# Performance work log

Hardware: AMD Instinct MI355X
Metric: run time of the kernel (lower is better)

Reference implementation:

```python
import jax, jax.numpy as jnp
import numpy as np

B, C, H, W = 2, 1024, 64, 64
E, TOP_K = 8, 2
FFN = C  # ffn_dim = in_channels; hidden_dim = out_channels = in_channels


def setup_inputs() -> dict:
    key = jax.random.key(0)
    ks = jax.random.split(key, 5)
    s = 0.02
    return {
        "hidden_states": jax.random.normal(ks[0], (B, C, H, W), jnp.float32),
        "gate_w": jax.random.normal(ks[1], (E, C), jnp.float32) * s,   # torch Linear weight [out,in]
        "w1": jax.random.normal(ks[2], (E, FFN, C), jnp.float32) * s,
        "w2": jax.random.normal(ks[3], (E, C, FFN), jnp.float32) * s,
        "w3": jax.random.normal(ks[4], (E, FFN, C), jnp.float32) * s,
    }


def reference(hidden_states, gate_w, w1, w2, w3):
    b, c = hidden_states.shape[0], hidden_states.shape[1]
    space = hidden_states.shape[2:]
    # (B, C, H, W) -> (B, H, W, C) -> (T, C)
    x = jnp.transpose(hidden_states, (0, 2, 3, 1)).reshape(-1, c)

    # Router: softmax in float32, top-k, renormalize (matches torch)
    logits = x @ gate_w.T                                   # [T, E]
    probs = jax.nn.softmax(logits.astype(jnp.float32), axis=-1)
    rw, sel = jax.lax.top_k(probs, TOP_K)                   # [T, K]
    rw = rw / jnp.sum(rw, axis=-1, keepdims=True)
    rw = rw.astype(x.dtype)

    # Combine weights per expert: zero where expert not selected -> exact
    # equivalence with gather/scatter dispatch (full capacity, no drops).
    combine = jnp.sum(jax.nn.one_hot(sel, E, dtype=x.dtype) * rw[..., None], axis=1)  # [T, E]

    out = jnp.zeros_like(x)
    for e in range(E):  # small fixed expert loop
        h = jax.nn.gelu(x @ w1[e].T, approximate=False) * (x @ w3[e].T)  # SwiGLU-style [T, FFN]
        out = out + combine[:, e:e + 1] * (h @ w2[e].T)

    out = out.reshape(b, *space, c)
    return jnp.transpose(out, (0, 3, 1, 2))  # (B, C, H, W)
```

## Files before the change

kernel.cpp:

```cpp
#include <hip/hip_runtime.h>
#include <hip/hip_bf16.h>
#include <math.h>

#define BB 2
#define CC 1024
#define HH 64
#define WW 64
#define HWH (HH*WW)
#define TT (BB*HWH)
#define EE 8
#define FFN 1024
#define MAXTILES 71
#define HCAP (MAXTILES*256)

typedef __bf16 bf16x8 __attribute__((ext_vector_type(8)));
typedef float  f32x4  __attribute__((ext_vector_type(4)));

__device__ __forceinline__ void gl_lds16(const __bf16* g, __bf16* l) {
    __builtin_amdgcn_global_load_lds(
        (const __attribute__((address_space(1))) void*)g,
        (__attribute__((address_space(3))) void*)l, 16, 0, 0);
}

__device__ __forceinline__ void barrier_raw() {
    asm volatile("" ::: "memory");
    __builtin_amdgcn_s_barrier();
    asm volatile("" ::: "memory");
}

__device__ __forceinline__ int xcd_swz(int orig, int nwg) {
    const int q = nwg >> 3, r = nwg & 7, x = orig & 7, o8 = orig >> 3;
    return (x < r ? x * (q + 1) : r * (q + 1) + (x - r) * q) + o8;
}

__device__ __forceinline__ float gelu_fast(float a) {
    const float a2 = a * a;
    const float t  = a * fmaf(0.044715f, a2, 1.0f);
    const float u  = __builtin_amdgcn_exp2f(t * -2.30220795f);
    return a * __builtin_amdgcn_rcpf(1.0f + u);
}

#define WAITV(N) asm volatile("s_waitcnt vmcnt(" #N ")" ::: "memory")
#define LGKM0()  asm volatile("s_waitcnt lgkmcnt(0)" ::: "memory")
#define SCHED0() __builtin_amdgcn_sched_barrier(0)
#define PRIO1()  __builtin_amdgcn_s_setprio(1)
#define PRIO0()  __builtin_amdgcn_s_setprio(0)

#define CVB 12288
#define XPB 8192
#define RTB 512
__global__ __launch_bounds__(256) void k_prep(
    const float* __restrict__ hs, const float* __restrict__ gate_w,
    const float* __restrict__ w1, const float* __restrict__ w2,
    const float* __restrict__ w3,
    __bf16* __restrict__ w1b, __bf16* __restrict__ w2b,
    __bf16* __restrict__ w3b, __bf16* __restrict__ X,
    float* __restrict__ logP) {
    __shared__ float sm[2112];
    const int bid = blockIdx.x;
    const int tid = threadIdx.x;

    if (bid < CVB) {
        const float* s; __bf16* d; int lb = bid;
        if (lb < 4096)      { s = w1; d = w1b; }
        else if (lb < 8192) { s = w2; d = w2b; lb -= 4096; }
        else                { s = w3; d = w3b; lb -= 8192; }
        const size_t i = (size_t)lb * 2048 + (size_t)tid * 8;
        const f32x4 v0 = *(const f32x4*)&s[i];
        const f32x4 v1 = *(const f32x4*)&s[i + 4];
        bf16x8 o;
#pragma unroll
        for (int j = 0; j < 4; ++j) { o[j] = (__bf16)v0[j]; o[4 + j] = (__bf16)v1[j]; }
        *(bf16x8*)&d[i] = o;
    } else if (bid < CVB + XPB) {
        const int lb  = bid - CVB;
        const int hw0 = (lb & 127) * 32;
        const int c0  = ((lb >> 7) & 31) * 32;
        const int b   = lb >> 12;
        float (*tile)[33] = (float(*)[33])sm;
        const int tx = tid & 31, ty = tid >> 5;
        const float* src = hs + ((size_t)b * CC + c0) * HWH + hw0;
#pragma unroll
        for (int i = 0; i < 4; ++i)
            tile[ty + i * 8][tx] = src[(size_t)(ty + i * 8) * HWH + tx];
        __syncthreads();
        __bf16* dst = X + ((size_t)b * HWH + hw0) * CC + c0;
#pragma unroll
        for (int i = 0; i < 4; ++i) {
            const int hwl = ty + i * 8;
            dst[(size_t)hwl * CC + tx] = (__bf16)tile[tx][hwl];
        }
    } else {
        const int lb  = bid - (CVB + XPB);
        const int q   = lb & 3;
        const int t64 = lb >> 2;
        float* g = sm;
        for (int i = tid; i < 2048; i += 256)
            g[i] = gate_w[(size_t)(i >> 8) * CC + q * 256 + (i & 255)];
        __syncthreads();
        const int q2 = tid >> 6, tl = tid & 63;
        const int t  = t64 * 64 + tl;
        const int b  = t >> 12, hw = t & 4095;
        const float* xp = hs + (size_t)b * CC * HWH + hw;
        float l[EE];
#pragma unroll
        for (int e = 0; e < EE; ++e) l[e] = 0.0f;
        const int cbase = q * 256 + q2 * 64;
        for (int c2 = 0; c2 < 64; ++c2) {
            const float xv = xp[(size_t)(cbase + c2) * HWH];
#pragma unroll
            for (int e = 0; e < EE; ++e) l[e] += xv * g[e * 256 + q2 * 64 + c2];
        }
        float* dst = logP + ((size_t)(q * 4 + q2) * TT + t) * 8;
        f32x4 a, c;
#pragma unroll
        for (int e = 0; e < 4; ++e) { a[e] = l[e]; c[e] = l[4 + e]; }
        *(f32x4*)dst = a;
        *(f32x4*)&dst[4] = c;
    }
}

__global__ __launch_bounds__(256) void k_top2(const float* __restrict__ logP,
                                              int* __restrict__ cnt,
                                              int* __restrict__ idxl,
                                              int* __restrict__ tokE,
                                              int* __restrict__ tokP,
                                              float* __restrict__ tokW) {
    __shared__ int lcnt[EE], lbase[EE];
    const int tid = threadIdx.x;
    const int t   = blockIdx.x * 256 + tid;
    if (tid < EE) lcnt[tid] = 0;
    __syncthreads();

    float l[EE];
#pragma unroll
    for (int e = 0; e < EE; ++e) l[e] = 0.0f;
#pragma unroll
    for (int pq = 0; pq < 16; ++pq) {
        const float* src = logP + ((size_t)pq * TT + t) * 8;
        const f32x4 a = *(const f32x4*)src;
        const f32x4 c = *(const f32x4*)&src[4];
#pragma unroll
        for (int e = 0; e < 4; ++e) { l[e] += a[e]; l[4 + e] += c[e]; }
    }

    int e1 = 0; float v1 = l[0];
#pragma unroll
    for (int e = 1; e < EE; ++e) { if (l[e] > v1) { v1 = l[e]; e1 = e; } }
    int e2 = -1; float v2 = -1e30f;
#pragma unroll
    for (int e = 0; e < EE; ++e) { if (e != e1 && l[e] > v2) { v2 = l[e]; e2 = e; } }

    const float p2 = __expf(v2 - v1);
    const float rs = 1.0f / (1.0f + p2);

    const int m1 = atomicAdd(&lcnt[e1], 1);
    const int m2 = atomicAdd(&lcnt[e2], 1);
    __syncthreads();
    if (tid < EE) lbase[tid] = atomicAdd(&cnt[tid], lcnt[tid]);
    __syncthreads();
    const int p1pos = lbase[e1] + m1;
    const int p2pos = lbase[e2] + m2;

    idxl[e1 * TT + p1pos] = t;
    idxl[e2 * TT + p2pos] = t;
    tokE[t] = e1 | (e2 << 8);
    tokP[2 * t]     = p1pos;
    tokP[2 * t + 1] = p2pos;
    tokW[2 * t]     = rs;
    tokW[2 * t + 1] = p2 * rs;
}

__global__ __launch_bounds__(512, 1)
void k_gemm1(const __bf16* __restrict__ X, const __bf16* __restrict__ w1b,
             const __bf16* __restrict__ w3b, const int* __restrict__ cnt,
             const int* __restrict__ idxl, __bf16* __restrict__ H) {
    const int lid = blockIdx.y * 8 + blockIdx.x;
    const int wg  = xcd_swz(lid, 8 * MAXTILES);
    const int n0  = (wg & 7) * 128;
    int ty = wg >> 3;
    int e = -1, mt = 0, goff = 0, acc_rows = 0;
#pragma unroll
    for (int ee = 0; ee < EE; ++ee) {
        const int me = (cnt[ee] + 255) >> 8;
        if (ty >= 0 && ty < me) { e = ee; mt = ty << 8; goff = acc_rows; }
        ty -= me;
        acc_rows += me << 8;
    }
    if (e < 0) return;
    const int cntE = cnt[e];
    const __bf16* W1 = w1b + (size_t)e * FFN * CC;
    const __bf16* W3 = w3b + (size_t)e * FFN * CC;

    __shared__ __align__(16) __bf16 sA[2][2][256 * 32];
    __shared__ __align__(16) __bf16 sB[2][2][256 * 32];

    const int tid  = threadIdx.x;
    const int lane = tid & 63, wave = tid >> 6;
    const int l15  = lane & 15, lq = lane >> 4;
    const int wm   = wave & 1;
    const int q    = wave >> 1;
    const int rsw  = (lq ^ ((l15 >> 1) & 3)) * 8;

    const int rl  = lane >> 2;
    const int csw = ((lane & 3) ^ ((rl >> 1) & 3)) * 8;

    int pr0 = mt + wave * 32 + rl;       if (pr0 > cntE - 1) pr0 = cntE - 1;
    int pr1 = mt + wave * 32 + 16 + rl;  if (pr1 > cntE - 1) pr1 = cntE - 1;
    const __bf16* gA0 = X + (size_t)idxl[e * TT + pr0] * CC + csw;
    const __bf16* gA1 = X + (size_t)idxl[e * TT + pr1] * CC + csw;
    const __bf16* WB = (wave & 1) ? W3 : W1;
    const __bf16* gB0 = WB + (size_t)(n0 + q * 32 + rl) * CC + csw;
    const __bf16* gB1 = WB + (size_t)(n0 + q * 32 + 16 + rl) * CC + csw;

    const int st0  = wave * 1024;
    const int aoff = (wm * 128 + l15) * 32 + rsw;
    const int boff = (q * 64 + l15) * 32 + rsw;

    f32x4 acc[8][4] = {};

#define G1_STGA(S, KS, KB) do {                                               \
    gl_lds16(gA0 + (KB) + (KS) * 32, &sA[S][KS][st0]);                        \
    gl_lds16(gA1 + (KB) + (KS) * 32, &sA[S][KS][st0 + 512]); } while (0)
#define G1_STGB(S, KS, KB) do {                                               \
    gl_lds16(gB0 + (KB) + (KS) * 32, &sB[S][KS][st0]);                        \
    gl_lds16(gB1 + (KB) + (KS) * 32, &sB[S][KS][st0 + 512]); } while (0)
#define G1_LDA(DST, S, KS, MF0)                                               \
    _Pragma("unroll") for (int mf_ = 0; mf_ < 4; ++mf_)                       \
        DST[mf_] = *(const bf16x8*)&sA[S][KS][aoff + (MF0 + mf_) * 512];
#define G1_LDB(DST, S, KS)                                                    \
    _Pragma("unroll") for (int nf_ = 0; nf_ < 4; ++nf_)                       \
        DST[nf_] = *(const bf16x8*)&sB[S][KS][boff + nf_ * 512];
#define G1_MM(M0, AF, BF)                                                     \
    _Pragma("unroll") for (int m_ = 0; m_ < 4; ++m_)                          \
    _Pragma("unroll") for (int n_ = 0; n_ < 4; ++n_)                          \
        acc[M0 + m_][n_] = __builtin_amdgcn_mfma_f32_16x16x32_bf16(           \
            AF[m_], BF[n_], acc[M0 + m_][n_], 0, 0, 0);

#define G1_TILE(S, KB, STG, LAST) do {                                        \
    bf16x8 af[4], bv[4];                                                      \
                                 \
    G1_LDA(af, S, 0, 0); G1_LDB(bv, S, 0);                                    \
    if (STG) G1_STGA((S) ^ 1, 0, KB);                                         \
    barrier_raw(); LGKM0(); SCHED0();                                         \
    PRIO1(); G1_MM(0, af, bv); PRIO0(); barrier_raw();                        \
                                               \
    G1_LDA(af, S, 0, 4);                                                      \
    if (STG) G1_STGB((S) ^ 1, 0, KB);                                         \
    if (LAST) { WAITV(0); } else { WAITV(4); }                                \
    barrier_raw(); LGKM0(); SCHED0();                                         \
    PRIO1(); G1_MM(4, af, bv); PRIO0(); barrier_raw();                        \
                                 \
    G1_LDA(af, S, 1, 0); G1_LDB(bv, S, 1);                                    \
    if (STG) G1_STGA((S) ^ 1, 1, KB);                                         \
    barrier_raw(); LGKM0(); SCHED0();                                         \
    PRIO1(); G1_MM(0, af, bv); PRIO0(); barrier_raw();                        \
                                               \
    G1_LDA(af, S, 1, 4);                                                      \
    if (STG) G1_STGB((S) ^ 1, 1, KB);                                         \
    if (!LAST) { WAITV(4); }                                                  \
    barrier_raw(); LGKM0(); SCHED0();                                         \
    PRIO1(); G1_MM(4, af, bv); PRIO0(); barrier_raw();                        \
} while (0)

    G1_STGA(0, 0, 0); G1_STGB(0, 0, 0); G1_STGA(0, 1, 0); G1_STGB(0, 1, 0);
    WAITV(0);
    barrier_raw();

    int kb = 64;
    for (int it = 0; it < 7; ++it) {
        G1_TILE(0, kb, 1, 0); kb += 64;
        G1_TILE(1, kb, 1, 0); kb += 64;
    }
    G1_TILE(0, kb, 1, 0);
    G1_TILE(1, 0, 0, 1);

#undef G1_STGA
#undef G1_STGB
#undef G1_LDA
#undef G1_LDB
#undef G1_MM
#undef G1_TILE

#pragma unroll
    for (int mf = 0; mf < 8; ++mf) {
        const int gr = goff + mt + wm * 128 + mf * 16 + lq * 4;
#pragma unroll
        for (int jp = 0; jp < 2; ++jp) {
            const int col = n0 + q * 32 + jp * 16 + l15;
#pragma unroll
            for (int r = 0; r < 4; ++r) {
                const float a  = acc[mf][jp][r];
                const float c  = acc[mf][jp + 2][r];
                H[(size_t)(gr + r) * FFN + col] = (__bf16)(gelu_fast(a) * c);
            }
        }
    }
}

__global__ __launch_bounds__(512, 1)
void k_gemm2(const __bf16* __restrict__ H, const __bf16* __restrict__ w2b,
             const int* __restrict__ cnt, __bf16* __restrict__ Z) {
    const int lid = blockIdx.y * 4 + blockIdx.x;
    const int wg  = xcd_swz(lid, 4 * MAXTILES);
    const int n0  = (wg & 3) * 256;
    int ty = wg >> 2;
    int e = -1, mt = 0, goff = 0, acc_rows = 0;
#pragma unroll
    for (int ee = 0; ee < EE; ++ee) {
        const int me = (cnt[ee] + 255) >> 8;
        if (ty >= 0 && ty < me) { e = ee; mt = ty << 8; goff = acc_rows; }
        ty -= me;
        acc_rows += me << 8;
    }
    if (e < 0) return;
    const __bf16* W2 = w2b + (size_t)e * CC * FFN;
    const __bf16* Ar = H + (size_t)(goff + mt) * FFN;

    __shared__ __align__(16) __bf16 sA[2][2][256 * 32];
    __shared__ __align__(16) __bf16 sB[2][2][256 * 32];

    const int tid  = threadIdx.x;
    const int lane = tid & 63, wave = tid >> 6;
    const int l15  = lane & 15, lq = lane >> 4;
    const int wm   = wave & 1;
    const int q    = wave >> 1;
    const int rsw  = (lq ^ ((l15 >> 1) & 3)) * 8;
    const int rl   = lane >> 2;
    const int csw  = ((lane & 3) ^ ((rl >> 1) & 3)) * 8;

    const __bf16* gA0 = Ar + (size_t)(wave * 32 + rl) * FFN + csw;
    const __bf16* gA1 = Ar + (size_t)(wave * 32 + 16 + rl) * FFN + csw;
    const __bf16* gB0 = W2 + (size_t)(n0 + wave * 32 + rl) * FFN + csw;
    const __bf16* gB1 = W2 + (size_t)(n0 + wave * 32 + 16 + rl) * FFN + csw;

    const int st0  = wave * 1024;
    const int aoff = (wm * 128 + l15) * 32 + rsw;
    const int boff = (q * 64 + l15) * 32 + rsw;

    f32x4 acc[8][4] = {};

#define G2_STGA(S, KS, KB) do {                                               \
    gl_lds16(gA0 + (KB) + (KS) * 32, &sA[S][KS][st0]);                        \
    gl_lds16(gA1 + (KB) + (KS) * 32, &sA[S][KS][st0 + 512]); } while (0)
#define G2_STGB(S, KS, KB) do {                                               \
    gl_lds16(gB0 + (KB) + (KS) * 32, &sB[S][KS][st0]);                        \
    gl_lds16(gB1 + (KB) + (KS) * 32, &sB[S][KS][st0 + 512]); } while (0)
#define G2_LDA(DST, S, KS, MF0)                                               \
    _Pragma("unroll") for (int mf_ = 0; mf_ < 4; ++mf_)                       \
        DST[mf_] = *(const bf16x8*)&sA[S][KS][aoff + (MF0 + mf_) * 512];
#define G2_LDB(DST, S, KS)                                                    \
    _Pragma("unroll") for (int nf_ = 0; nf_ < 4; ++nf_)                       \
        DST[nf_] = *(const bf16x8*)&sB[S][KS][boff + nf_ * 512];
#define G2_MM(M0, AF, BF)                                                     \
    _Pragma("unroll") for (int m_ = 0; m_ < 4; ++m_)                          \
    _Pragma("unroll") for (int n_ = 0; n_ < 4; ++n_)                          \
        acc[M0 + m_][n_] = __builtin_amdgcn_mfma_f32_16x16x32_bf16(           \
            AF[m_], BF[n_], acc[M0 + m_][n_], 0, 0, 0);

#define G2_TILE(S, KB, STG, LAST) do {                                        \
    bf16x8 af[4], bv[4];                                                      \
    G2_LDA(af, S, 0, 0); G2_LDB(bv, S, 0);                                    \
    if (STG) G2_STGA((S) ^ 1, 0, KB);                                         \
    barrier_raw(); LGKM0(); SCHED0();                                         \
    PRIO1(); G2_MM(0, af, bv); PRIO0(); barrier_raw();                        \
    G2_LDA(af, S, 0, 4);                                                      \
    if (STG) G2_STGB((S) ^ 1, 0, KB);                                         \
    if (LAST) { WAITV(0); } else { WAITV(4); }                                \
    barrier_raw(); LGKM0(); SCHED0();                                         \
    PRIO1(); G2_MM(4, af, bv); PRIO0(); barrier_raw();                        \
    G2_LDA(af, S, 1, 0); G2_LDB(bv, S, 1);                                    \
    if (STG) G2_STGA((S) ^ 1, 1, KB);                                         \
    barrier_raw(); LGKM0(); SCHED0();                                         \
    PRIO1(); G2_MM(0, af, bv); PRIO0(); barrier_raw();                        \
    G2_LDA(af, S, 1, 4);                                                      \
    if (STG) G2_STGB((S) ^ 1, 1, KB);                                         \
    if (!LAST) { WAITV(4); }                                                  \
    barrier_raw(); LGKM0(); SCHED0();                                         \
    PRIO1(); G2_MM(4, af, bv); PRIO0(); barrier_raw();                        \
} while (0)

    G2_STGA(0, 0, 0); G2_STGB(0, 0, 0); G2_STGA(0, 1, 0); G2_STGB(0, 1, 0);
    WAITV(0);
    barrier_raw();

    int kb = 64;
    for (int it = 0; it < 7; ++it) {
        G2_TILE(0, kb, 1, 0); kb += 64;
        G2_TILE(1, kb, 1, 0); kb += 64;
    }
    G2_TILE(0, kb, 1, 0);
    G2_TILE(1, 0, 0, 1);

#undef G2_STGA
#undef G2_STGB
#undef G2_LDA
#undef G2_LDB
#undef G2_MM
#undef G2_TILE

#pragma unroll
    for (int mf = 0; mf < 8; ++mf) {
        const int gr = goff + mt + wm * 128 + mf * 16 + lq * 4;
#pragma unroll
        for (int nf = 0; nf < 4; ++nf) {
            const int col = n0 + q * 64 + nf * 16 + l15;
#pragma unroll
            for (int r = 0; r < 4; ++r)
                Z[(size_t)(gr + r) * CC + col] = (__bf16)acc[mf][nf][r];
        }
    }
}

__global__ __launch_bounds__(256) void k_combine(const __bf16* __restrict__ Z,
                                                 const int* __restrict__ cnt,
                                                 const int* __restrict__ tokE,
                                                 const int* __restrict__ tokP,
                                                 const float* __restrict__ tokW,
                                                 float* __restrict__ out) {
    __shared__ float tile[32][33];
    __shared__ int s_pre[EE];
    const int tid = threadIdx.x;
    if (tid < EE) {
        int a = 0;
        for (int ee = 0; ee < tid; ++ee) a += ((cnt[ee] + 255) >> 8) << 8;
        s_pre[tid] = a;
    }
    __syncthreads();

    const int t0 = blockIdx.x * 32;
    const int c0 = blockIdx.y * 32;
    const int tx = tid & 31;
    const int ty = tid >> 5;

#pragma unroll
    for (int i = 0; i < 4; ++i) {
        const int tl = ty + 8 * i;
        const int t  = t0 + tl;
        const int ee = tokE[t];
        const int e1 = ee & 0xff, e2 = ee >> 8;
        const int r1 = s_pre[e1] + tokP[2 * t];
        const int r2 = s_pre[e2] + tokP[2 * t + 1];
        const float v = tokW[2 * t]     * (float)Z[(size_t)r1 * CC + c0 + tx]
                      + tokW[2 * t + 1] * (float)Z[(size_t)r2 * CC + c0 + tx];
        tile[tl][tx] = v;
    }
    __syncthreads();

    const int b   = t0 >> 12;
    const int hw0 = t0 & 4095;
#pragma unroll
    for (int i = 0; i < 4; ++i) {
        const int cl = ty + 8 * i;
        out[(size_t)b * CC * HWH + (size_t)(c0 + cl) * HWH + hw0 + tx] = tile[tx][cl];
    }
}

extern "C" void kernel_launch(void* const* d_in, const int* in_sizes, int n_in,
                              void* d_out, int out_size, void* d_ws, size_t ws_size,
                              hipStream_t stream) {
    const float* hs     = (const float*)d_in[0];
    const float* gate_w = (const float*)d_in[1];
    const float* w1     = (const float*)d_in[2];
    const float* w2     = (const float*)d_in[3];
    const float* w3     = (const float*)d_in[4];
    float* out = (float*)d_out;

    const size_t WSZ = (size_t)EE * FFN * CC * 2;
    char* ws = (char*)d_ws;
    __bf16* w2b  = (__bf16*)ws;
    __bf16* w1b  = (__bf16*)(ws + WSZ);
    __bf16* w3b  = (__bf16*)(ws + 2 * WSZ);
    __bf16* X    = (__bf16*)(ws + 3 * WSZ);
    __bf16* Zbuf = (__bf16*)(ws + WSZ);
    __bf16* Hbuf = (__bf16*)(ws + 4 * WSZ);
    float*  logP = (float*)Hbuf;
    char* p = ws + 4 * WSZ + (size_t)HCAP * FFN * 2;
    int*   idxl  = (int*)p;           p += (size_t)EE * TT * 4;
    int*   tokE  = (int*)p;           p += (size_t)TT * 4;
    int*   tokP  = (int*)p;           p += (size_t)2 * TT * 4;
    float* tokW  = (float*)p;         p += (size_t)2 * TT * 4;
    int*   cnt   = (int*)p;           p += 256;

    hipMemsetAsync(cnt, 0, EE * sizeof(int), stream);

    k_prep<<<CVB + XPB + RTB, 256, 0, stream>>>(
        hs, gate_w, w1, w2, w3, w1b, w2b, w3b, X, logP);
    k_top2<<<TT / 256, 256, 0, stream>>>(logP, cnt, idxl, tokE, tokP, tokW);

    k_gemm1<<<dim3(FFN / 128, MAXTILES), 512, 0, stream>>>(
        X, w1b, w3b, cnt, idxl, Hbuf);
    k_gemm2<<<dim3(CC / 256, MAXTILES), 512, 0, stream>>>(
        Hbuf, w2b, cnt, Zbuf);
    k_combine<<<dim3(TT / 32, CC / 32), 256, 0, stream>>>(
        Zbuf, cnt, tokE, tokP, tokW, out);
}
```

Measured before the change: 355.3 us.

## Shrink GEMM tiles, use triple-buffered K=32 pipeline, raise occupancy to 4 blocks

Both expert GEMMs switch from 256x256 tiles with 64-wide K double-buffering to 256x128 tiles with a 32-wide K step and a three-stage LDS ring buffer. Each K-step needs only one barrier instead of eight, and launch bounds now allow four 512-thread blocks per CU, so more waves can hide latency. The grids double in the N dimension, giving more blocks. The cost is lower arithmetic intensity per tile, more redundant reloads of the A and B operands, and tighter register budgets.

```diff
diff --git a/kernel.cpp b/kernel.cpp
--- a/kernel.cpp
+++ b/kernel.cpp
@@ -171,10 +171,108 @@
     tokW[2 * t + 1] = p2 * rs;
 }
 
-__global__ __launch_bounds__(512, 1)
+#define GT_TILE(SR, SS, KB, STG, WC) do {                                     \
+    if (STG) {                                                                \
+        gl_lds16(gA0 + (KB), &sA[SS][stA]);                                   \
+        gl_lds16(gA1 + (KB), &sA[SS][stA + 4096]);                            \
+        gl_lds16(gB0 + (KB), &sB[SS][stA]);                                   \
+    }                                                                         \
+    bf16x8 af[4], bv[4];                                                      \
+    _Pragma("unroll") for (int f_ = 0; f_ < 4; ++f_) {                        \
+        af[f_] = *(const bf16x8*)&sA[SR][aoff + f_ * 512];                    \
+        bv[f_] = *(const bf16x8*)&sB[SR][boff + f_ * 512];                    \
+    }                                                                         \
+    LGKM0(); SCHED0();                                                        \
+    PRIO1();                                                                  \
+    _Pragma("unroll") for (int m_ = 0; m_ < 4; ++m_)                          \
+    _Pragma("unroll") for (int n_ = 0; n_ < 4; ++n_)                          \
+        acc[m_][n_] = __builtin_amdgcn_mfma_f32_16x16x32_bf16(                \
+            af[m_], bv[n_], acc[m_][n_], 0, 0, 0);                            \
+    PRIO0();                                                                  \
+    WC;                                                                       \
+    barrier_raw();                                                            \
+} while (0)
+
+__global__ __launch_bounds__(512, 4)
 void k_gemm1(const __bf16* __restrict__ X, const __bf16* __restrict__ w1b,
              const __bf16* __restrict__ w3b, const int* __restrict__ cnt,
              const int* __restrict__ idxl, __bf16* __restrict__ H) {
+    const int lid = blockIdx.y * 16 + blockIdx.x;
+    const int wg  = xcd_swz(lid, 16 * MAXTILES);
+    const int n0  = (wg & 15) * 64;
+    int ty = wg >> 4;
+    int e = -1, mt = 0, goff = 0, acc_rows = 0;
+#pragma unroll
+    for (int ee = 0; ee < EE; ++ee) {
+        const int me = (cnt[ee] + 255) >> 8;
+        if (ty >= 0 && ty < me) { e = ee; mt = ty << 8; goff = acc_rows; }
+        ty -= me;
+        acc_rows += me << 8;
+    }
+    if (e < 0) return;
+    const int cntE = cnt[e];
+    const __bf16* W1 = w1b + (size_t)e * FFN * CC;
+    const __bf16* W3 = w3b + (size_t)e * FFN * CC;
+
+    __shared__ __align__(16) __bf16 sA[3][8192];
+    __shared__ __align__(16) __bf16 sB[3][4096];
+
+    const int tid  = threadIdx.x;
+    const int lane = tid & 63, wave = tid >> 6;
+    const int l15  = lane & 15, lq = lane >> 4;
+    const int wm   = wave & 3;
+    const int wq   = wave >> 2;
+    const int rsw  = (lq ^ ((l15 >> 1) & 3)) * 8;
+
+    const int csw  = ((tid & 3) ^ ((tid >> 3) & 3)) * 8;
+    const int cswb = ((lane & 3) ^ ((lane >> 3) & 3)) * 8;
+
+    int pr0 = mt + (tid >> 2);        if (pr0 > cntE - 1) pr0 = cntE - 1;
+    int pr1 = mt + 128 + (tid >> 2);  if (pr1 > cntE - 1) pr1 = cntE - 1;
+    const __bf16* gA0 = X + (size_t)idxl[e * TT + pr0] * CC + csw;
+    const __bf16* gA1 = X + (size_t)idxl[e * TT + pr1] * CC + csw;
+    const __bf16* WB  = (wave & 1) ? W3 : W1;
+    const __bf16* gB0 = WB + (size_t)(n0 + (wave >> 1) * 16 + (lane >> 2)) * CC + cswb;
+
+    const int stA  = wave * 512;
+    const int aoff = (wm * 64 + l15) * 32 + rsw;
+    const int boff = (wq * 64 + l15) * 32 + rsw;
+
+    f32x4 acc[4][4] = {};
+
+    gl_lds16(gA0,      &sA[0][stA]); gl_lds16(gA1,      &sA[0][stA + 4096]);
+    gl_lds16(gB0,      &sB[0][stA]);
+    gl_lds16(gA0 + 32, &sA[1][stA]); gl_lds16(gA1 + 32, &sA[1][stA + 4096]);
+    gl_lds16(gB0 + 32, &sB[1][stA]);
+    WAITV(3);
+    barrier_raw();
+
+    int kb = 64;
+    for (int it = 0; it < 10; ++it) {
+        GT_TILE(0, 2, kb, 1, WAITV(3)); kb += 32;
+        GT_TILE(1, 0, kb, 1, WAITV(3)); kb += 32;
+        GT_TILE(2, 1, kb, 1, WAITV(3)); kb += 32;
+    }
+    GT_TILE(0, 0, 0, 0, WAITV(0));
+    GT_TILE(1, 0, 0, 0, (void)0);
+
+#pragma unroll
+    for (int mf = 0; mf < 4; ++mf) {
+        const int gr  = goff + mt + wm * 64 + mf * 16 + lq * 4;
+        const int col = n0 + wq * 32 + l15;
+#pragma unroll
+        for (int r = 0; r < 4; ++r) {
+            const float a0 = acc[mf][0][r], c0 = acc[mf][1][r];
+            const float a1 = acc[mf][2][r], c1 = acc[mf][3][r];
+            H[(size_t)(gr + r) * FFN + col]      = (__bf16)(gelu_fast(a0) * c0);
+            H[(size_t)(gr + r) * FFN + col + 16] = (__bf16)(gelu_fast(a1) * c1);
+        }
+    }
+}
+
+__global__ __launch_bounds__(512, 4)
+void k_gemm2(const __bf16* __restrict__ H, const __bf16* __restrict__ w2b,
+             const int* __restrict__ cnt, __bf16* __restrict__ Z) {
     const int lid = blockIdx.y * 8 + blockIdx.x;
     const int wg  = xcd_swz(lid, 8 * MAXTILES);
     const int n0  = (wg & 7) * 128;
@@ -188,223 +286,53 @@
         acc_rows += me << 8;
     }
     if (e < 0) return;
-    const int cntE = cnt[e];
-    const __bf16* W1 = w1b + (size_t)e * FFN * CC;
-    const __bf16* W3 = w3b + (size_t)e * FFN * CC;
-
-    __shared__ __align__(16) __bf16 sA[2][2][256 * 32];
-    __shared__ __align__(16) __bf16 sB[2][2][256 * 32];
+    const __bf16* W2 = w2b + (size_t)e * CC * FFN;
+    const __bf16* Ar = H + (size_t)(goff + mt) * FFN;
+
+    __shared__ __align__(16) __bf16 sA[3][8192];
+    __shared__ __align__(16) __bf16 sB[3][4096];
 
     const int tid  = threadIdx.x;
     const int lane = tid & 63, wave = tid >> 6;
     const int l15  = lane & 15, lq = lane >> 4;
-    const int wm   = wave & 1;
-    const int q    = wave >> 1;
+    const int wm   = wave & 3;
+    const int wq   = wave >> 2;
     const int rsw  = (lq ^ ((l15 >> 1) & 3)) * 8;
-
-    const int rl  = lane >> 2;
-    const int csw = ((lane & 3) ^ ((rl >> 1) & 3)) * 8;
-
-    int pr0 = mt + wave * 32 + rl;       if (pr0 > cntE - 1) pr0 = cntE - 1;
-    int pr1 = mt + wave * 32 + 16 + rl;  if (pr1 > cntE - 1) pr1 = cntE - 1;
-    const __bf16* gA0 = X + (size_t)idxl[e * TT + pr0] * CC + csw;
-    const __bf16* gA1 = X + (size_t)idxl[e * TT + pr1] * CC + csw;
-    const __bf16* WB = (wave & 1) ? W3 : W1;
-    const __bf16* gB0 = WB + (size_t)(n0 + q * 32 + rl) * CC + csw;
-    const __bf16* gB1 = WB + (size_t)(n0 + q * 32 + 16 + rl) * CC + csw;
-
-    const int st0  = wave * 1024;
-    const int aoff = (wm * 128 + l15) * 32 + rsw;
-    const int boff = (q * 64 + l15) * 32 + rsw;
-
-    f32x4 acc[8][4] = {};
-
-#define G1_STGA(S, KS, KB) do {                                               \
-    gl_lds16(gA0 + (KB) + (KS) * 32, &sA[S][KS][st0]);                        \
-    gl_lds16(gA1 + (KB) + (KS) * 32, &sA[S][KS][st0 + 512]); } while (0)
-#define G1_STGB(S, KS, KB) do {                                               \
-    gl_lds16(gB0 + (KB) + (KS) * 32, &sB[S][KS][st0]);                        \
-    gl_lds16(gB1 + (KB) + (KS) * 32, &sB[S][KS][st0 + 512]); } while (0)
-#define G1_LDA(DST, S, KS, MF0)                                               \
-    _Pragma("unroll") for (int mf_ = 0; mf_ < 4; ++mf_)                       \
-        DST[mf_] = *(const bf16x8*)&sA[S][KS][aoff + (MF0 + mf_) * 512];
-#define G1_LDB(DST, S, KS)                                                    \
-    _Pragma("unroll") for (int nf_ = 0; nf_ < 4; ++nf_)                       \
-        DST[nf_] = *(const bf16x8*)&sB[S][KS][boff + nf_ * 512];
-#define G1_MM(M0, AF, BF)                                                     \
-    _Pragma("unroll") for (int m_ = 0; m_ < 4; ++m_)                          \
-    _Pragma("unroll") for (int n_ = 0; n_ < 4; ++n_)                          \
-        acc[M0 + m_][n_] = __builtin_amdgcn_mfma_f32_16x16x32_bf16(           \
-            AF[m_], BF[n_], acc[M0 + m_][n_], 0, 0, 0);
-
-#define G1_TILE(S, KB, STG, LAST) do {                                        \
-    bf16x8 af[4], bv[4];                                                      \
-                                 \
-    G1_LDA(af, S, 0, 0); G1_LDB(bv, S, 0);                                    \
-    if (STG) G1_STGA((S) ^ 1, 0, KB);                                         \
-    barrier_raw(); LGKM0(); SCHED0();                                         \
-    PRIO1(); G1_MM(0, af, bv); PRIO0(); barrier_raw();                        \
-                                               \
-    G1_LDA(af, S, 0, 4);                                                      \
-    if (STG) G1_STGB((S) ^ 1, 0, KB);                                         \
-    if (LAST) { WAITV(0); } else { WAITV(4); }                                \
-    barrier_raw(); LGKM0(); SCHED0();                                         \
-    PRIO1(); G1_MM(4, af, bv); PRIO0(); barrier_raw();                        \
-                                 \
-    G1_LDA(af, S, 1, 0); G1_LDB(bv, S, 1);                                    \
-    if (STG) G1_STGA((S) ^ 1, 1, KB);                                         \
-    barrier_raw(); LGKM0(); SCHED0();                                         \
-    PRIO1(); G1_MM(0, af, bv); PRIO0(); barrier_raw();                        \
-                                               \
-    G1_LDA(af, S, 1, 4);                                                      \
-    if (STG) G1_STGB((S) ^ 1, 1, KB);                                         \
-    if (!LAST) { WAITV(4); }                                                  \
-    barrier_raw(); LGKM0(); SCHED0();                                         \
-    PRIO1(); G1_MM(4, af, bv); PRIO0(); barrier_raw();                        \
-} while (0)
-
-    G1_STGA(0, 0, 0); G1_STGB(0, 0, 0); G1_STGA(0, 1, 0); G1_STGB(0, 1, 0);
-    WAITV(0);
+    const int csw  = ((tid & 3) ^ ((tid >> 3) & 3)) * 8;
+    const int cswb = ((lane & 3) ^ ((lane >> 3) & 3)) * 8;
+
+    const __bf16* gA0 = Ar + (size_t)(tid >> 2) * FFN + csw;
+    const __bf16* gA1 = Ar + (size_t)(128 + (tid >> 2)) * FFN + csw;
+    const __bf16* gB0 = W2 + (size_t)(n0 + wave * 16 + (lane >> 2)) * FFN + cswb;
+
+    const int stA  = wave * 512;
+    const int aoff = (wm * 64 + l15) * 32 + rsw;
+    const int boff = (wq * 64 + l15) * 32 + rsw;
+
+    f32x4 acc[4][4] = {};
+
+    gl_lds16(gA0,      &sA[0][stA]); gl_lds16(gA1,      &sA[0][stA + 4096]);
+    gl_lds16(gB0,      &sB[0][stA]);
+    gl_lds16(gA0 + 32, &sA[1][stA]); gl_lds16(gA1 + 32, &sA[1][stA + 4096]);
+    gl_lds16(gB0 + 32, &sB[1][stA]);
+    WAITV(3);
     barrier_raw();
 
     int kb = 64;
-    for (int it = 0; it < 7; ++it) {
-        G1_TILE(0, kb, 1, 0); kb += 64;
-        G1_TILE(1, kb, 1, 0); kb += 64;
-    }
-    G1_TILE(0, kb, 1, 0);
-    G1_TILE(1, 0, 0, 1);
-
-#undef G1_STGA
-#undef G1_STGB
-#undef G1_LDA
-#undef G1_LDB
-#undef G1_MM
-#undef G1_TILE
-
-#pragma unroll
-    for (int mf = 0; mf < 8; ++mf) {
-        const int gr = goff + mt + wm * 128 + mf * 16 + lq * 4;
-#pragma unroll
-        for (int jp = 0; jp < 2; ++jp) {
-            const int col = n0 + q * 32 + jp * 16 + l15;
-#pragma unroll
-            for (int r = 0; r < 4; ++r) {
-                const float a  = acc[mf][jp][r];
-                const float c  = acc[mf][jp + 2][r];
-                H[(size_t)(gr + r) * FFN + col] = (__bf16)(gelu_fast(a) * c);
-            }
-        }
-    }
-}
-
-__global__ __launch_bounds__(512, 1)
-void k_gemm2(const __bf16* __restrict__ H, const __bf16* __restrict__ w2b,
-             const int* __restrict__ cnt, __bf16* __restrict__ Z) {
-    const int lid = blockIdx.y * 4 + blockIdx.x;
-    const int wg  = xcd_swz(lid, 4 * MAXTILES);
-    const int n0  = (wg & 3) * 256;
-    int ty = wg >> 2;
-    int e = -1, mt = 0, goff = 0, acc_rows = 0;
-#pragma unroll
-    for (int ee = 0; ee < EE; ++ee) {
-        const int me = (cnt[ee] + 255) >> 8;
-        if (ty >= 0 && ty < me) { e = ee; mt = ty << 8; goff = acc_rows; }
-        ty -= me;
-        acc_rows += me << 8;
-    }
-    if (e < 0) return;
-    const __bf16* W2 = w2b + (size_t)e * CC * FFN;
-    const __bf16* Ar = H + (size_t)(goff + mt) * FFN;
-
-    __shared__ __align__(16) __bf16 sA[2][2][256 * 32];
-    __shared__ __align__(16) __bf16 sB[2][2][256 * 32];
-
-    const int tid  = threadIdx.x;
-    const int lane = tid & 63, wave = tid >> 6;
-    const int l15  = lane & 15, lq = lane >> 4;
-    const int wm   = wave & 1;
-    const int q    = wave >> 1;
-    const int rsw  = (lq ^ ((l15 >> 1) & 3)) * 8;
-    const int rl   = lane >> 2;
-    const int csw  = ((lane & 3) ^ ((rl >> 1) & 3)) * 8;
-
-    const __bf16* gA0 = Ar + (size_t)(wave * 32 + rl) * FFN + csw;
-    const __bf16* gA1 = Ar + (size_t)(wave * 32 + 16 + rl) * FFN + csw;
-    const __bf16* gB0 = W2 + (size_t)(n0 + wave * 32 + rl) * FFN + csw;
-    const __bf16* gB1 = W2 + (size_t)(n0 + wave * 32 + 16 + rl) * FFN + csw;
-
-    const int st0  = wave * 1024;
-    const int aoff = (wm * 128 + l15) * 32 + rsw;
-    const int boff = (q * 64 + l15) * 32 + rsw;
-
-    f32x4 acc[8][4] = {};
-
-#define G2_STGA(S, KS, KB) do {                                               \
-    gl_lds16(gA0 + (KB) + (KS) * 32, &sA[S][KS][st0]);                        \
-    gl_lds16(gA1 + (KB) + (KS) * 32, &sA[S][KS][st0 + 512]); } while (0)
-#define G2_STGB(S, KS, KB) do {                                               \
-    gl_lds16(gB0 + (KB) + (KS) * 32, &sB[S][KS][st0]);                        \
-    gl_lds16(gB1 + (KB) + (KS) * 32, &sB[S][KS][st0 + 512]); } while (0)
-#define G2_LDA(DST, S, KS, MF0)                                               \
-    _Pragma("unroll") for (int mf_ = 0; mf_ < 4; ++mf_)                       \
-        DST[mf_] = *(const bf16x8*)&sA[S][KS][aoff + (MF0 + mf_) * 512];
-#define G2_LDB(DST, S, KS)                                                    \
-    _Pragma("unroll") for (int nf_ = 0; nf_ < 4; ++nf_)                       \
-        DST[nf_] = *(const bf16x8*)&sB[S][KS][boff + nf_ * 512];
-#define G2_MM(M0, AF, BF)                                                     \
-    _Pragma("unroll") for (int m_ = 0; m_ < 4; ++m_)                          \
-    _Pragma("unroll") for (int n_ = 0; n_ < 4; ++n_)                          \
-        acc[M0 + m_][n_] = __builtin_amdgcn_mfma_f32_16x16x32_bf16(           \
-            AF[m_], BF[n_], acc[M0 + m_][n_], 0, 0, 0);
-
-#define G2_TILE(S, KB, STG, LAST) do {                                        \
-    bf16x8 af[4], bv[4];                                                      \
-    G2_LDA(af, S, 0, 0); G2_LDB(bv, S, 0);                                    \
-    if (STG) G2_STGA((S) ^ 1, 0, KB);                                         \
-    barrier_raw(); LGKM0(); SCHED0();                                         \
-    PRIO1(); G2_MM(0, af, bv); PRIO0(); barrier_raw();                        \
-    G2_LDA(af, S, 0, 4);                                                      \
-    if (STG) G2_STGB((S) ^ 1, 0, KB);                                         \
-    if (LAST) { WAITV(0); } else { WAITV(4); }                                \
-    barrier_raw(); LGKM0(); SCHED0();                                         \
-    PRIO1(); G2_MM(4, af, bv); PRIO0(); barrier_raw();                        \
-    G2_LDA(af, S, 1, 0); G2_LDB(bv, S, 1);                                    \
-    if (STG) G2_STGA((S) ^ 1, 1, KB);                                         \
-    barrier_raw(); LGKM0(); SCHED0();                                         \
-    PRIO1(); G2_MM(0, af, bv); PRIO0(); barrier_raw();                        \
-    G2_LDA(af, S, 1, 4);                                                      \
-    if (STG) G2_STGB((S) ^ 1, 1, KB);                                         \
-    if (!LAST) { WAITV(4); }                                                  \
-    barrier_raw(); LGKM0(); SCHED0();                                         \
-    PRIO1(); G2_MM(4, af, bv); PRIO0(); barrier_raw();                        \
-} while (0)
-
-    G2_STGA(0, 0, 0); G2_STGB(0, 0, 0); G2_STGA(0, 1, 0); G2_STGB(0, 1, 0);
-    WAITV(0);
-    barrier_raw();
-
-    int kb = 64;
-    for (int it = 0; it < 7; ++it) {
-        G2_TILE(0, kb, 1, 0); kb += 64;
-        G2_TILE(1, kb, 1, 0); kb += 64;
-    }
-    G2_TILE(0, kb, 1, 0);
-    G2_TILE(1, 0, 0, 1);
-
-#undef G2_STGA
-#undef G2_STGB
-#undef G2_LDA
-#undef G2_LDB
-#undef G2_MM
-#undef G2_TILE
-
-#pragma unroll
-    for (int mf = 0; mf < 8; ++mf) {
-        const int gr = goff + mt + wm * 128 + mf * 16 + lq * 4;
+    for (int it = 0; it < 10; ++it) {
+        GT_TILE(0, 2, kb, 1, WAITV(3)); kb += 32;
+        GT_TILE(1, 0, kb, 1, WAITV(3)); kb += 32;
+        GT_TILE(2, 1, kb, 1, WAITV(3)); kb += 32;
+    }
+    GT_TILE(0, 0, 0, 0, WAITV(0));
+    GT_TILE(1, 0, 0, 0, (void)0);
+
+#pragma unroll
+    for (int mf = 0; mf < 4; ++mf) {
+        const int gr = goff + mt + wm * 64 + mf * 16 + lq * 4;
 #pragma unroll
         for (int nf = 0; nf < 4; ++nf) {
-            const int col = n0 + q * 64 + nf * 16 + l15;
+            const int col = n0 + wq * 64 + nf * 16 + l15;
 #pragma unroll
             for (int r = 0; r < 4; ++r)
                 Z[(size_t)(gr + r) * CC + col] = (__bf16)acc[mf][nf][r];
@@ -488,9 +416,9 @@
         hs, gate_w, w1, w2, w3, w1b, w2b, w3b, X, logP);
     k_top2<<<TT / 256, 256, 0, stream>>>(logP, cnt, idxl, tokE, tokP, tokW);
 
-    k_gemm1<<<dim3(FFN / 128, MAXTILES), 512, 0, stream>>>(
+    k_gemm1<<<dim3(FFN / 64, MAXTILES), 512, 0, stream>>>(
         X, w1b, w3b, cnt, idxl, Hbuf);
-    k_gemm2<<<dim3(CC / 256, MAXTILES), 512, 0, stream>>>(
+    k_gemm2<<<dim3(CC / 128, MAXTILES), 512, 0, stream>>>(
         Hbuf, w2b, cnt, Zbuf);
     k_combine<<<dim3(TT / 32, CC / 32), 256, 0, stream>>>(
         Zbuf, cnt, tokE, tokP, tokW, out);
```

New measurement: 329.8 us. -7.2%, faster.
